# Performance work log

Measured on AMD Instinct MI355X. Metric: run time of the kernel, lower is better.

## Reference

```python
import jax, jax.numpy as jnp
import numpy as np

B, S, D_IN, D_OUT, H = 4, 2048, 1024, 1024, 16
HD = D_OUT // H  # head_dim = 64


def setup_inputs() -> dict:
    key = jax.random.key(0)
    ks = jax.random.split(key, 6)
    scale = 1.0 / np.sqrt(D_IN)
    return {
        "x": jax.random.normal(ks[0], (B, S, D_IN), dtype=jnp.float32),
        "Wq": jax.random.normal(ks[1], (D_IN, D_OUT), dtype=jnp.float32) * scale,
        "Wk": jax.random.normal(ks[2], (D_IN, D_OUT), dtype=jnp.float32) * scale,
        "Wv": jax.random.normal(ks[3], (D_IN, D_OUT), dtype=jnp.float32) * scale,
        "Wo": jax.random.normal(ks[4], (D_OUT, D_OUT), dtype=jnp.float32) * (1.0 / np.sqrt(D_OUT)),
        "bo": jax.random.normal(ks[5], (D_OUT,), dtype=jnp.float32) * 0.02,
    }


def reference(x, Wq, Wk, Wv, Wo, bo):
    b, n, _ = x.shape
    h, hd = H, HD
    # projections -> (b, h, n, hd)
    q = (x @ Wq).reshape(b, n, h, hd).transpose(0, 2, 1, 3)
    k = (x @ Wk).reshape(b, n, h, hd).transpose(0, 2, 1, 3)
    v = (x @ Wv).reshape(b, n, h, hd).transpose(0, 2, 1, 3)
    # scores (b, h, n, n) with causal mask then scale (matches original order)
    scores = jnp.einsum("bhqd,bhkd->bhqk", q, k)
    causal = jnp.tril(jnp.ones((n, n), dtype=bool))  # True = keep
    scores = jnp.where(causal, scores, -jnp.inf) / jnp.sqrt(jnp.asarray(hd, x.dtype))
    attn = jax.nn.softmax(scores, axis=-1)
    ctx = jnp.einsum("bhqk,bhkd->bhqd", attn, v)
    ctx = ctx.transpose(0, 2, 1, 3).reshape(b, n, h * hd)
    return ctx @ Wo + bo
```

## Files before the change

kernel.cpp:

```cpp
#include <hip/hip_runtime.h>
#include <hip/hip_bf16.h>
#include <math.h>

typedef __attribute__((ext_vector_type(4))) float f32x4;
typedef __attribute__((ext_vector_type(16))) float f32x16;
typedef __attribute__((ext_vector_type(8))) short bf16x8;
typedef __attribute__((ext_vector_type(4))) unsigned int u32x4;

#define DEV __device__ __forceinline__
#define MFMA16 __builtin_amdgcn_mfma_f32_16x16x32_bf16
#define MFMA32 __builtin_amdgcn_mfma_f32_32x32x16_bf16
#define SBAR __builtin_amdgcn_s_barrier()
#define SCHED0 __builtin_amdgcn_sched_barrier(0)

constexpr int S      = 2048;
constexpr int DMODEL = 1024;
constexpr int HD     = 64;
constexpr int MROWS  = 4 * 2048;

DEV unsigned short f2bf(float f) {
  union { float f; unsigned int u; } v; v.f = f;
  unsigned int u = v.u;
  unsigned int r = u + 0x7fffu + ((u >> 16) & 1u);
  return (unsigned short)(r >> 16);
}

DEV unsigned int pkbf(float lo, float hi) {
  unsigned int r;
  asm("v_cvt_pk_bf16_f32 %0, %1, %2" : "=v"(r) : "v"(lo), "v"(hi));
  return r;
}

DEV float fexp2(float x) { return __builtin_amdgcn_exp2f(x); }

DEV void gload_lds16(const void* g, void* l) {
  __builtin_amdgcn_global_load_lds(
      (const __attribute__((address_space(1))) unsigned int*)g,
      (__attribute__((address_space(3))) unsigned int*)l, 16, 0, 0);
}

__global__ __launch_bounds__(256) void k_conv(const float* __restrict__ in,
                                              unsigned short* __restrict__ out) {
  int i = blockIdx.x * 256 + threadIdx.x;
  float4 v = ((const float4*)in)[i];
  ushort4 o;
  o.x = f2bf(v.x); o.y = f2bf(v.y); o.z = f2bf(v.z); o.w = f2bf(v.w);
  ((ushort4*)out)[i] = o;
}

__global__ __launch_bounds__(256) void k_transpose4(const float* __restrict__ Wq,
                                                    const float* __restrict__ Wk,
                                                    const float* __restrict__ Wv,
                                                    const float* __restrict__ Wo,
                                                    unsigned short* __restrict__ wt,
                                                    unsigned short* __restrict__ wot) {
  __shared__ float tile[32][33];
  const int z = blockIdx.z;
  const float* W = (z == 0) ? Wq : (z == 1) ? Wk : (z == 2) ? Wv : Wo;
  unsigned short* Wt = (z == 3) ? wot : wt + (size_t)z * DMODEL * DMODEL;
  int n0 = blockIdx.x * 32, k0 = blockIdx.y * 32;
  int tx = threadIdx.x, ty = threadIdx.y;
#pragma unroll
  for (int j = 0; j < 4; ++j)
    tile[ty + j * 8][tx] = W[(size_t)(k0 + ty + j * 8) * DMODEL + n0 + tx];
  __syncthreads();
#pragma unroll
  for (int j = 0; j < 4; ++j)
    Wt[(size_t)(n0 + ty + j * 8) * DMODEL + k0 + tx] = f2bf(tile[tx][ty + j * 8]);
}

template<int NBX, int EPI>
__global__ __launch_bounds__(512, 2) void k_gemm8(const unsigned short* __restrict__ A,
                                                  const unsigned short* __restrict__ Bt,
                                                  unsigned short* __restrict__ Qg,
                                                  unsigned short* __restrict__ Kg,
                                                  unsigned short* __restrict__ Vg,
                                                  const float* __restrict__ bo,
                                                  float* __restrict__ out) {
  __shared__ __align__(16) char lds[98304];
  const int tid = threadIdx.x, lane = tid & 63;
  const int wid = tid >> 6, wm = wid >> 1, wn = wid & 1;
  const int lq = lane & 15, lg = lane >> 4;
  const int flat = blockIdx.x;
  const int wg = (flat & 7) * (NBX * 4) + (flat >> 3);
  const int by = wg / NBX, bx = wg % NBX;
  const int m0 = by * 256, n0 = bx * 128;

  auto stage = [&](int kt, int buf) {
    char* dA = lds + buf * 49152;
    char* dB = dA + 32768;
    const unsigned short* gA = A + (size_t)m0 * DMODEL + kt * 64;
    const unsigned short* gB = Bt + (size_t)n0 * DMODEL + kt * 64;
#pragma unroll
    for (int i = 0; i < 4; ++i) {
      int c = tid + i * 512; int r = c >> 3, cc = c & 7;
      gload_lds16(gA + (size_t)r * DMODEL + ((cc ^ (r & 7)) << 3), dA + c * 16);
    }
#pragma unroll
    for (int i = 0; i < 2; ++i) {
      int c = tid + i * 512; int r = c >> 3, cc = c & 7;
      gload_lds16(gB + (size_t)r * DMODEL + ((cc ^ (r & 7)) << 3), dB + c * 16);
    }
  };

  stage(0, 0);
  stage(1, 1);
  SCHED0;
  asm volatile("s_waitcnt vmcnt(6)" ::: "memory");
  SCHED0;
  SBAR;
  SCHED0;

  f32x4 acc[4][4] = {};
#pragma unroll 1
  for (int t = 0; t < 16; ++t) {
    const int cur = t & 1;
    const char* pA = lds + cur * 49152;
    const char* pB = pA + 32768;
    bf16x8 af[4][2], bf[4][2];
#pragma unroll
    for (int kk = 0; kk < 2; ++kk) {
#pragma unroll
      for (int mi = 0; mi < 4; ++mi) {
        int row = wm * 64 + mi * 16 + lq;
        af[mi][kk] = *(const bf16x8*)(pA + row * 128 + ((((kk << 2) + lg) ^ (row & 7)) << 4));
      }
#pragma unroll
      for (int ni = 0; ni < 4; ++ni) {
        int row = wn * 64 + ni * 16 + lq;
        bf[ni][kk] = *(const bf16x8*)(pB + row * 128 + ((((kk << 2) + lg) ^ (row & 7)) << 4));
      }
    }
    asm volatile("s_waitcnt lgkmcnt(0)" ::: "memory");
    SCHED0;
    SBAR;
    SCHED0;
    if (t < 14) stage(t + 2, cur);
    __builtin_amdgcn_s_setprio(1);
#pragma unroll
    for (int kk = 0; kk < 2; ++kk)
#pragma unroll
      for (int mi = 0; mi < 4; ++mi)
#pragma unroll
        for (int ni = 0; ni < 4; ++ni)
          acc[mi][ni] = MFMA16(af[mi][kk], bf[ni][kk], acc[mi][ni], 0, 0, 0);
    __builtin_amdgcn_s_setprio(0);
    SCHED0;
    if (t < 14) {
      asm volatile("s_waitcnt vmcnt(6)" ::: "memory");
    } else if (t == 14) {
      asm volatile("s_waitcnt vmcnt(0)" ::: "memory");
    }
    SCHED0;
    SBAR;
    SCHED0;
  }

  if (EPI == 0) {
#pragma unroll
    for (int mi = 0; mi < 4; ++mi)
#pragma unroll
      for (int ni = 0; ni < 4; ++ni) {
        int n = n0 + wn * 64 + ni * 16 + lq;
        int widx = n >> 10, nn = n & 1023;
        int h = nn >> 6, d = nn & 63;
        unsigned short* dst = (widx == 0) ? Qg : ((widx == 1) ? Kg : Vg);
        float scale = (widx == 0) ? 0.18033688f : 1.0f;
#pragma unroll
        for (int r = 0; r < 4; ++r) {
          int m = m0 + wm * 64 + mi * 16 + lg * 4 + r;
          int b_ = m >> 11, s_ = m & 2047;
          dst[(size_t)((b_ * 16 + h) * 2048 + s_) * HD + d] = f2bf(acc[mi][ni][r] * scale);
        }
      }
  } else {
#pragma unroll
    for (int mi = 0; mi < 4; ++mi)
#pragma unroll
      for (int ni = 0; ni < 4; ++ni) {
        int n = n0 + wn * 64 + ni * 16 + lq;
        float bv = bo[n];
#pragma unroll
        for (int r = 0; r < 4; ++r) {
          int m = m0 + wm * 64 + mi * 16 + lg * 4 + r;
          out[(size_t)m * DMODEL + n] = acc[mi][ni][r] + bv;
        }
      }
  }
}

__global__ __launch_bounds__(512, 2) void k_attn(const unsigned short* __restrict__ Qg,
                                                 const unsigned short* __restrict__ Kg,
                                                 const unsigned short* __restrict__ Vg,
                                                 unsigned short* __restrict__ Ctx) {
  __shared__ __align__(16) char lds[32768];
  const int f = blockIdx.x;
  const int i4 = f & 255, hi2 = f >> 8;
  const int bh = i4 >> 2, q = i4 & 3;
  const int Qb = hi2 ? (7 - q) : q;
  const int tid = threadIdx.x;
  const int lane = tid & 63, w = tid >> 6;
  const int lq5 = lane & 31, hi = lane >> 5;
  const size_t base = (size_t)bh * (S * HD);
  const int b = bh >> 4, h = bh & 15;
  const int vkrow = tid >> 3, vcc = tid & 7;

  const int q0w = Qb * 256 + w * 32;
  const int tmax = 4 * Qb + 3;
  const int diag = q0w >> 6;

  bf16x8 qF[4];
#pragma unroll
  for (int dc = 0; dc < 4; ++dc)
    qF[dc] = *(const bf16x8*)(Qg + base + (size_t)(q0w + lq5) * HD + dc * 16 + hi * 8);

  f32x16 o0 = {}, o1 = {};
  float m_run = -INFINITY, l_run = 0.f;

  {
    int row = tid >> 3, cc = tid & 7, scc = cc ^ (row & 7);
    gload_lds16(Kg + base + (size_t)row * HD + scc * 8, lds + tid * 16);
    bf16x8 vv = *(const bf16x8*)(Vg + base + (size_t)vkrow * HD + vcc * 8);
#pragma unroll
    for (int j = 0; j < 8; ++j) {
      int d = vcc * 8 + j;
      int fd = (d & 7) ^ ((d >> 3) & 7);
      *(unsigned short*)(lds + 16384 + d * 128 + (((vkrow >> 3) ^ fd) << 4) + (vkrow & 7) * 2) =
          (unsigned short)vv[j];
    }
  }
  __syncthreads();

#pragma unroll 1
  for (int t = 0; t <= tmax; ++t) {
    const int cur = t & 1, nxt = cur ^ 1;
    char* sK  = lds + cur * 8192;
    char* sVT = lds + 16384 + cur * 8192;
    const bool have_next = (t < tmax);
    bf16x8 vv;
    if (have_next) {
      vv = *(const bf16x8*)(Vg + base + (size_t)((t + 1) * 64 + vkrow) * HD + vcc * 8);
      int row = tid >> 3, cc = tid & 7, scc = cc ^ (row & 7);
      gload_lds16(Kg + base + (size_t)((t + 1) * 64 + row) * HD + scc * 8,
                  lds + nxt * 8192 + tid * 16);
    }
    const bool active = (t <= diag);
    if (active) {
      const bool isdiag = (t == diag);
      const int nkb = (isdiag && !(q0w & 32)) ? 1 : 2;
      f32x16 st0 = {}, st1 = {};
#pragma unroll
      for (int dc = 0; dc < 4; ++dc) {
        int row = lq5;
        bf16x8 a0 = *(const bf16x8*)(sK + row * 128 + (((2 * dc + hi) ^ (row & 7)) << 4));
        st0 = MFMA32(a0, qF[dc], st0, 0, 0, 0);
      }
      if (nkb == 2) {
#pragma unroll
        for (int dc = 0; dc < 4; ++dc) {
          int row = 32 + lq5;
          bf16x8 a1 = *(const bf16x8*)(sK + row * 128 + (((2 * dc + hi) ^ (row & 7)) << 4));
          st1 = MFMA32(a1, qF[dc], st1, 0, 0, 0);
        }
      }
      if (isdiag) {
        int qo = q0w + lq5 - t * 64;
        if (q0w & 32) {
#pragma unroll
          for (int r = 0; r < 16; ++r) {
            int key = 32 + (r & 3) + 8 * (r >> 2) + 4 * hi;
            st1[r] = (key > qo) ? -INFINITY : st1[r];
          }
        } else {
#pragma unroll
          for (int r = 0; r < 16; ++r) {
            int key = (r & 3) + 8 * (r >> 2) + 4 * hi;
            st0[r] = (key > qo) ? -INFINITY : st0[r];
          }
        }
      }
      float mx = st0[0];
#pragma unroll
      for (int r = 1; r < 16; ++r) mx = fmaxf(mx, st0[r]);
      if (nkb == 2) {
#pragma unroll
        for (int r = 0; r < 16; ++r) mx = fmaxf(mx, st1[r]);
      }
      mx = fmaxf(mx, __shfl_xor(mx, 32));
      bool need = !(mx <= m_run + 8.0f);
      if (__any(need)) {
        float mn = fmaxf(m_run, mx);
        float alpha = fexp2(m_run - mn);
        m_run = mn;
        l_run *= alpha;
#pragma unroll
        for (int r = 0; r < 16; ++r) { o0[r] *= alpha; o1[r] *= alpha; }
      }
      float rs[4] = {0.f, 0.f, 0.f, 0.f};
#pragma unroll
      for (int r = 0; r < 16; ++r) {
        float p = fexp2(st0[r] - m_run);
        st0[r] = p;
        rs[r & 3] += p;
      }
      if (nkb == 2) {
#pragma unroll
        for (int r = 0; r < 16; ++r) {
          float p = fexp2(st1[r] - m_run);
          st1[r] = p;
          rs[r & 3] += p;
        }
      }
      float rsum = (rs[0] + rs[1]) + (rs[2] + rs[3]);
      rsum += __shfl_xor(rsum, 32);
      l_run += rsum;
      {
        unsigned int wv[8];
#pragma unroll
        for (int j = 0; j < 8; ++j) wv[j] = pkbf(st0[2 * j], st0[2 * j + 1]);
        asm("v_permlane32_swap_b32 %0, %1" : "+v"(wv[0]), "+v"(wv[2]));
        asm("v_permlane32_swap_b32 %0, %1" : "+v"(wv[1]), "+v"(wv[3]));
        asm("v_permlane32_swap_b32 %0, %1" : "+v"(wv[4]), "+v"(wv[6]));
        asm("v_permlane32_swap_b32 %0, %1" : "+v"(wv[5]), "+v"(wv[7]));
        union { bf16x8 v; unsigned int u[4]; } fa, fb;
        fa.u[0] = wv[0]; fa.u[1] = wv[1]; fa.u[2] = wv[2]; fa.u[3] = wv[3];
        fb.u[0] = wv[4]; fb.u[1] = wv[5]; fb.u[2] = wv[6]; fb.u[3] = wv[7];
#pragma unroll
        for (int kc = 0; kc < 2; ++kc) {
          bf16x8 bp = kc ? fb.v : fa.v;
          {
            int d = lq5, fd = (d & 7) ^ ((d >> 3) & 7);
            bf16x8 av = *(const bf16x8*)(sVT + d * 128 + (((kc * 2 + hi) ^ fd) << 4));
            o0 = MFMA32(av, bp, o0, 0, 0, 0);
          }
          {
            int d = 32 + lq5, fd = (d & 7) ^ ((d >> 3) & 7);
            bf16x8 av = *(const bf16x8*)(sVT + d * 128 + (((kc * 2 + hi) ^ fd) << 4));
            o1 = MFMA32(av, bp, o1, 0, 0, 0);
          }
        }
      }
      if (nkb == 2) {
        unsigned int wv[8];
#pragma unroll
        for (int j = 0; j < 8; ++j) wv[j] = pkbf(st1[2 * j], st1[2 * j + 1]);
        asm("v_permlane32_swap_b32 %0, %1" : "+v"(wv[0]), "+v"(wv[2]));
        asm("v_permlane32_swap_b32 %0, %1" : "+v"(wv[1]), "+v"(wv[3]));
        asm("v_permlane32_swap_b32 %0, %1" : "+v"(wv[4]), "+v"(wv[6]));
        asm("v_permlane32_swap_b32 %0, %1" : "+v"(wv[5]), "+v"(wv[7]));
        union { bf16x8 v; unsigned int u[4]; } fa, fb;
        fa.u[0] = wv[0]; fa.u[1] = wv[1]; fa.u[2] = wv[2]; fa.u[3] = wv[3];
        fb.u[0] = wv[4]; fb.u[1] = wv[5]; fb.u[2] = wv[6]; fb.u[3] = wv[7];
#pragma unroll
        for (int kc = 0; kc < 2; ++kc) {
          bf16x8 bp = kc ? fb.v : fa.v;
          {
            int d = lq5, fd = (d & 7) ^ ((d >> 3) & 7);
            bf16x8 av = *(const bf16x8*)(sVT + d * 128 + ((((2 + kc) * 2 + hi) ^ fd) << 4));
            o0 = MFMA32(av, bp, o0, 0, 0, 0);
          }
          {
            int d = 32 + lq5, fd = (d & 7) ^ ((d >> 3) & 7);
            bf16x8 av = *(const bf16x8*)(sVT + d * 128 + ((((2 + kc) * 2 + hi) ^ fd) << 4));
            o1 = MFMA32(av, bp, o1, 0, 0, 0);
          }
        }
      }
    }
    if (have_next) {
      char* dVT = lds + 16384 + nxt * 8192;
#pragma unroll
      for (int j = 0; j < 8; ++j) {
        int d = vcc * 8 + j;
        int fd = (d & 7) ^ ((d >> 3) & 7);
        *(unsigned short*)(dVT + d * 128 + (((vkrow >> 3) ^ fd) << 4) + (vkrow & 7) * 2) =
            (unsigned short)vv[j];
      }
    }
    __syncthreads();
  }

  __syncthreads();
  {
    float inv = 1.0f / l_run;
    char* slice = lds + w * 4096;
#pragma unroll
    for (int db = 0; db < 2; ++db)
#pragma unroll
      for (int j = 0; j < 8; ++j) {
        int d0 = (j & 1) * 2 + (j >> 1) * 8 + 4 * hi + 32 * db;
        float va = (db ? o1[2 * j] : o0[2 * j]) * inv;
        float vb = (db ? o1[2 * j + 1] : o0[2 * j + 1]) * inv;
        *(unsigned int*)(slice + lq5 * 128 + (((d0 >> 3) ^ (lq5 & 7)) << 4) + (d0 & 7) * 2) =
            pkbf(va, vb);
      }
    asm volatile("s_waitcnt lgkmcnt(0)" ::: "memory");
#pragma unroll
    for (int i = 0; i < 4; ++i) {
      int r = lane >> 1, cc = (lane & 1) * 4 + i;
      u32x4 v = *(const u32x4*)(slice + r * 128 + ((cc ^ (r & 7)) << 4));
      *(u32x4*)(Ctx + (size_t)(b * S + q0w + r) * DMODEL + h * HD + cc * 8) = v;
    }
  }
}

extern "C" void kernel_launch(void* const* d_in, const int* in_sizes, int n_in,
                              void* d_out, int out_size, void* d_ws, size_t ws_size,
                              hipStream_t stream) {
  const float* x  = (const float*)d_in[0];
  const float* Wq = (const float*)d_in[1];
  const float* Wk = (const float*)d_in[2];
  const float* Wv = (const float*)d_in[3];
  const float* Wo = (const float*)d_in[4];
  const float* bo = (const float*)d_in[5];
  float* out = (float*)d_out;

  char* p = (char*)d_ws;
  unsigned short* xb  = (unsigned short*)p; p += (size_t)MROWS * DMODEL * 2;
  unsigned short* wt  = (unsigned short*)p; p += (size_t)3 * DMODEL * DMODEL * 2;
  unsigned short* wot = (unsigned short*)p; p += (size_t)DMODEL * DMODEL * 2;
  unsigned short* qg  = (unsigned short*)p; p += (size_t)MROWS * DMODEL * 2;
  unsigned short* kg  = (unsigned short*)p; p += (size_t)MROWS * DMODEL * 2;
  unsigned short* vg  = (unsigned short*)p; p += (size_t)MROWS * DMODEL * 2;
  unsigned short* ctx = (unsigned short*)p; p += (size_t)MROWS * DMODEL * 2;

  k_conv<<<(MROWS * DMODEL) / 1024, 256, 0, stream>>>(x, xb);
  k_transpose4<<<dim3(32, 32, 4), dim3(32, 8), 0, stream>>>(Wq, Wk, Wv, Wo, wt, wot);
  k_gemm8<24, 0><<<768, 512, 0, stream>>>(xb, wt, qg, kg, vg, nullptr, nullptr);
  k_attn<<<512, 512, 0, stream>>>(qg, kg, vg, ctx);
  k_gemm8<8, 1><<<256, 512, 0, stream>>>(ctx, wot, nullptr, nullptr, nullptr, bo, out);
}
```

Before: 178.2 us.

## Store V pre-transposed from QKV GEMM and async-load it into LDS

The QKV projection epilogue now writes V in a per-head transposed (d-major, sequence-contiguous) layout using 4-wide vector stores. The attention kernel can then load V tiles straight into LDS with the same direct global-to-LDS path used for K, instead of loading V into registers and scattering 2-byte LDS writes to transpose it. This removes the per-iteration register round trip and scalar LDS stores and lets the V load overlap like the K load. The cost is strided 8-byte global writes in the GEMM epilogue for the V third of the output.

```diff
diff --git a/kernel.cpp b/kernel.cpp
--- a/kernel.cpp
+++ b/kernel.cpp
@@ -74,7 +74,7 @@
                                                   const unsigned short* __restrict__ Bt,
                                                   unsigned short* __restrict__ Qg,
                                                   unsigned short* __restrict__ Kg,
-                                                  unsigned short* __restrict__ Vg,
+                                                  unsigned short* __restrict__ Vt,
                                                   const float* __restrict__ bo,
                                                   float* __restrict__ out) {
   __shared__ __align__(16) char lds[98304];
@@ -164,13 +164,21 @@
         int n = n0 + wn * 64 + ni * 16 + lq;
         int widx = n >> 10, nn = n & 1023;
         int h = nn >> 6, d = nn & 63;
-        unsigned short* dst = (widx == 0) ? Qg : ((widx == 1) ? Kg : Vg);
-        float scale = (widx == 0) ? 0.18033688f : 1.0f;
-#pragma unroll
-        for (int r = 0; r < 4; ++r) {
-          int m = m0 + wm * 64 + mi * 16 + lg * 4 + r;
-          int b_ = m >> 11, s_ = m & 2047;
-          dst[(size_t)((b_ * 16 + h) * 2048 + s_) * HD + d] = f2bf(acc[mi][ni][r] * scale);
+        int mbase = m0 + wm * 64 + mi * 16 + lg * 4;
+        int b_ = mbase >> 11, s_ = mbase & 2047;
+        if (widx == 2) {
+          ushort4 o;
+          o.x = f2bf(acc[mi][ni][0]);
+          o.y = f2bf(acc[mi][ni][1]);
+          o.z = f2bf(acc[mi][ni][2]);
+          o.w = f2bf(acc[mi][ni][3]);
+          *(ushort4*)(Vt + ((size_t)((b_ * 16 + h) * 64 + d)) * S + s_) = o;
+        } else {
+          unsigned short* dst = (widx == 0) ? Qg : Kg;
+          float scale = (widx == 0) ? 0.18033688f : 1.0f;
+#pragma unroll
+          for (int r = 0; r < 4; ++r)
+            dst[(size_t)((b_ * 16 + h) * 2048 + s_ + r) * HD + d] = f2bf(acc[mi][ni][r] * scale);
         }
       }
   } else {
@@ -191,7 +199,7 @@
 
 __global__ __launch_bounds__(512, 2) void k_attn(const unsigned short* __restrict__ Qg,
                                                  const unsigned short* __restrict__ Kg,
-                                                 const unsigned short* __restrict__ Vg,
+                                                 const unsigned short* __restrict__ Vt,
                                                  unsigned short* __restrict__ Ctx) {
   __shared__ __align__(16) char lds[32768];
   const int f = blockIdx.x;
@@ -203,7 +211,11 @@
   const int lq5 = lane & 31, hi = lane >> 5;
   const size_t base = (size_t)bh * (S * HD);
   const int b = bh >> 4, h = bh & 15;
-  const int vkrow = tid >> 3, vcc = tid & 7;
+  const int krow = tid >> 3, kcc = tid & 7, scc = kcc ^ (krow & 7);
+  const int vd = tid >> 3;
+  const int vfd = (vd & 7) ^ ((vd >> 3) & 7);
+  const int vscc = (tid & 7) ^ vfd;
+  const unsigned short* VtRow = Vt + (size_t)(bh * 64 + vd) * S;
 
   const int q0w = Qb * 256 + w * 32;
   const int tmax = 4 * Qb + 3;
@@ -217,18 +229,8 @@
   f32x16 o0 = {}, o1 = {};
   float m_run = -INFINITY, l_run = 0.f;
 
-  {
-    int row = tid >> 3, cc = tid & 7, scc = cc ^ (row & 7);
-    gload_lds16(Kg + base + (size_t)row * HD + scc * 8, lds + tid * 16);
-    bf16x8 vv = *(const bf16x8*)(Vg + base + (size_t)vkrow * HD + vcc * 8);
-#pragma unroll
-    for (int j = 0; j < 8; ++j) {
-      int d = vcc * 8 + j;
-      int fd = (d & 7) ^ ((d >> 3) & 7);
-      *(unsigned short*)(lds + 16384 + d * 128 + (((vkrow >> 3) ^ fd) << 4) + (vkrow & 7) * 2) =
-          (unsigned short)vv[j];
-    }
-  }
+  gload_lds16(Kg + base + (size_t)krow * HD + scc * 8, lds + tid * 16);
+  gload_lds16(VtRow + vscc * 8, lds + 16384 + tid * 16);
   __syncthreads();
 
 #pragma unroll 1
@@ -237,12 +239,11 @@
     char* sK  = lds + cur * 8192;
     char* sVT = lds + 16384 + cur * 8192;
     const bool have_next = (t < tmax);
-    bf16x8 vv;
     if (have_next) {
-      vv = *(const bf16x8*)(Vg + base + (size_t)((t + 1) * 64 + vkrow) * HD + vcc * 8);
-      int row = tid >> 3, cc = tid & 7, scc = cc ^ (row & 7);
-      gload_lds16(Kg + base + (size_t)((t + 1) * 64 + row) * HD + scc * 8,
+      gload_lds16(Kg + base + (size_t)((t + 1) * 64 + krow) * HD + scc * 8,
                   lds + nxt * 8192 + tid * 16);
+      gload_lds16(VtRow + (t + 1) * 64 + vscc * 8,
+                  lds + 16384 + nxt * 8192 + tid * 16);
     }
     const bool active = (t <= diag);
     if (active) {
@@ -365,16 +366,6 @@
             o1 = MFMA32(av, bp, o1, 0, 0, 0);
           }
         }
-      }
-    }
-    if (have_next) {
-      char* dVT = lds + 16384 + nxt * 8192;
-#pragma unroll
-      for (int j = 0; j < 8; ++j) {
-        int d = vcc * 8 + j;
-        int fd = (d & 7) ^ ((d >> 3) & 7);
-        *(unsigned short*)(dVT + d * 128 + (((vkrow >> 3) ^ fd) << 4) + (vkrow & 7) * 2) =
-            (unsigned short)vv[j];
       }
     }
     __syncthreads();
@@ -421,12 +412,12 @@
   unsigned short* wot = (unsigned short*)p; p += (size_t)DMODEL * DMODEL * 2;
   unsigned short* qg  = (unsigned short*)p; p += (size_t)MROWS * DMODEL * 2;
   unsigned short* kg  = (unsigned short*)p; p += (size_t)MROWS * DMODEL * 2;
-  unsigned short* vg  = (unsigned short*)p; p += (size_t)MROWS * DMODEL * 2;
+  unsigned short* vt  = (unsigned short*)p; p += (size_t)MROWS * DMODEL * 2;
   unsigned short* ctx = (unsigned short*)p; p += (size_t)MROWS * DMODEL * 2;
 
   k_conv<<<(MROWS * DMODEL) / 1024, 256, 0, stream>>>(x, xb);
   k_transpose4<<<dim3(32, 32, 4), dim3(32, 8), 0, stream>>>(Wq, Wk, Wv, Wo, wt, wot);
-  k_gemm8<24, 0><<<768, 512, 0, stream>>>(xb, wt, qg, kg, vg, nullptr, nullptr);
-  k_attn<<<512, 512, 0, stream>>>(qg, kg, vg, ctx);
+  k_gemm8<24, 0><<<768, 512, 0, stream>>>(xb, wt, qg, kg, vt, nullptr, nullptr);
+  k_attn<<<512, 512, 0, stream>>>(qg, kg, vt, ctx);
   k_gemm8<8, 1><<<256, 512, 0, stream>>>(ctx, wot, nullptr, nullptr, nullptr, bo, out);
 }
```

New measurement: 166.1 us. 6.8% less time.
